# Kernel optimization log

Measured on AMD Instinct MI355X. Metric: run time of the kernel, lower is better.

## Reference

```python
import jax, jax.numpy as jnp
import numpy as np

K = 20
EPS = 1e-5
NEG_SLOPE = 0.2


def _knn_idx(x, k):
    # x: (B, N, C). Torch: pd = -||xi||^2 + 2 xi.xj - ||xj||^2, topk largest = nearest.
    inner = jnp.einsum('bnc,bmc->bnm', x, x)
    xx = jnp.sum(x * x, axis=-1)  # (B, N)
    pd = 2.0 * inner - xx[:, :, None] - xx[:, None, :]
    _, idx = jax.lax.top_k(pd, k)  # (B, N, k)
    return idx


def _bn_lrelu(h, gamma, beta, axes):
    mean = jnp.mean(h, axis=axes)
    var = jnp.var(h, axis=axes)  # biased, as in torch BN training normalization
    hn = (h - mean) * jax.lax.rsqrt(var + EPS) * gamma + beta
    return jnp.where(hn >= 0, hn, NEG_SLOPE * hn)


def _edge_conv(x, W, gamma, beta, k):
    # x: (B, N, C); W: (O, 2C). Returns (B, N, O).
    idx = _knn_idx(x, k)
    nbr = jax.vmap(lambda xb, ib: xb[ib])(x, idx)  # (B, N, k, C) gather
    center = jnp.broadcast_to(x[:, :, None, :], nbr.shape)
    edge = jnp.concatenate([nbr - center, center], axis=-1)  # (B, N, k, 2C)
    h = jnp.einsum('bnkc,oc->bnko', edge, W)
    h = _bn_lrelu(h, gamma, beta, axes=(0, 1, 2))
    return jnp.max(h, axis=2)  # max over k -> (B, N, O)


def setup_inputs() -> dict:
    key = jax.random.key(0)
    ks = jax.random.split(key, 16)
    B, N = 32, 1024
    d = {'x': jax.random.normal(ks[0], (B, N, 3), dtype=jnp.float32)}
    dims = [(64, 6), (64, 128), (128, 128), (256, 256), (1024, 512)]
    for i, (o, c) in enumerate(dims, start=1):
        d[f'W{i}'] = jax.random.normal(ks[i], (o, c), dtype=jnp.float32) * 0.05
        d[f'g{i}'] = jnp.ones((o,), dtype=jnp.float32)
        d[f'b{i}'] = jnp.zeros((o,), dtype=jnp.float32)
    return d


def reference(x, W1, g1, b1, W2, g2, b2, W3, g3, b3, W4, g4, b4, W5, g5, b5):
    B = x.shape[0]
    x1 = _edge_conv(x, W1, g1, b1, K)    # (B, N, 64)
    x2 = _edge_conv(x1, W2, g2, b2, K)   # (B, N, 64)
    x3 = _edge_conv(x2, W3, g3, b3, K)   # (B, N, 128)
    x4 = _edge_conv(x3, W4, g4, b4, K)   # (B, N, 256)
    cat = jnp.concatenate([x1, x2, x3, x4], axis=-1)  # (B, N, 512)
    h = jnp.einsum('bnc,oc->bno', cat, W5)            # (B, N, 1024)
    h = _bn_lrelu(h, g5, b5, axes=(0, 1))
    out = jnp.max(h, axis=1)  # adaptive max pool over points -> (B, 1024)
    return out.reshape(B, 1, -1)
```

## Files before the change

### kernel.cpp

```cpp
#include <hip/hip_runtime.h>
#include <math.h>

#define BB 32
#define NN 1024
#define KNNK 20
#define PTS (BB*NN)

typedef __attribute__((ext_vector_type(8)))  short short8;
typedef __attribute__((ext_vector_type(4)))  float f32x4;
typedef __attribute__((ext_vector_type(16))) float f32x16;

__device__ __forceinline__ float lrelu(float v){ return v >= 0.f ? v : 0.2f*v; }

__device__ __forceinline__ unsigned short f2b(float x){
    union { float f; unsigned u; } c; c.f = x;
    unsigned r = c.u + 0x7FFFu + ((c.u >> 16) & 1u);
    return (unsigned short)(r >> 16);
}

__global__ void sq_kernel(const float* __restrict__ x, int stride, int C, float* __restrict__ xx){
    int pn = blockIdx.x*256 + threadIdx.x;
    if (pn >= PTS) return;
    const float* r = x + (size_t)pn*stride;
    float s = 0.f;
    if ((C & 3) == 0){
        for (int c = 0; c < C; c += 4){
            float4 v = *(const float4*)&r[c];
            s = fmaf(v.x, v.x, s); s = fmaf(v.y, v.y, s);
            s = fmaf(v.z, v.z, s); s = fmaf(v.w, v.w, s);
        }
    } else {
        for (int c = 0; c < C; ++c){ float v = r[c]; s = fmaf(v, v, s); }
    }
    xx[pn] = s;
}

template<int C>
__global__ void __launch_bounds__(512, 4) knn_kernel(const float* __restrict__ x, int stride,
                                                     const float* __restrict__ xx,
                                                     int* __restrict__ idxout){
    constexpr int KC = 8;
    __shared__ __align__(16) float Bs[2][NN][4];
    __shared__ float xs[NN];
    int bid = (int)blockIdx.x;
    bid = (bid & 7)*128 + (bid >> 3);
    const int b  = bid >> 5;
    const int rb = bid & 31;
    const int r0 = rb * 32;
    const int tid = threadIdx.x;
    const int wv = tid >> 6, lane = tid & 63;
    const float* xb = x + (size_t)b*NN*stride;

    if (tid < 256) *(float4*)&xs[tid*4] = *(const float4*)&xx[b*NN + tid*4];

    float acc[4][16];
    #pragma unroll
    for (int r=0;r<4;++r)
        #pragma unroll
        for (int q=0;q<16;++q) acc[r][q] = 0.f;

    const int wrow = wv*4;

    #pragma unroll 1
    for (int kc = 0; kc < C; kc += KC){
        __syncthreads();
        #pragma unroll
        for (int ps = 0; ps < 4; ++ps){
            int i = tid + ps*512;
            int col = i >> 1, half = i & 1;
            float4 v;
            if constexpr (C == 3){
                float vv[4];
                #pragma unroll
                for (int j = 0; j < 4; ++j){
                    int k = half*4 + j;
                    vv[j] = (k < 3) ? xb[(size_t)col*3 + k] : 0.f;
                }
                v = make_float4(vv[0], vv[1], vv[2], vv[3]);
            } else {
                v = *(const float4*)&xb[(size_t)col*stride + kc + half*4];
            }
            *(float4*)&Bs[half][col][0] = v;
        }
        __syncthreads();
        #pragma unroll
        for (int s = 0; s < 2; ++s){
            float4 ar[4];
            #pragma unroll
            for (int r=0;r<4;++r)
                ar[r] = *(const float4*)&Bs[s][r0 + wrow + r][0];
            #pragma unroll
            for (int q=0;q<16;++q){
                float4 bv = *(const float4*)&Bs[s][lane + 64*q][0];
                #pragma unroll
                for (int r=0;r<4;++r){
                    acc[r][q] = fmaf(ar[r].x, bv.x, acc[r][q]);
                    acc[r][q] = fmaf(ar[r].y, bv.y, acc[r][q]);
                    acc[r][q] = fmaf(ar[r].z, bv.z, acc[r][q]);
                    acc[r][q] = fmaf(ar[r].w, bv.w, acc[r][q]);
                }
            }
        }
    }

    const unsigned long long lt = (lane == 0) ? 0ull : ((~0ull) >> (64 - lane));
    #pragma unroll
    for (int r = 0; r < 4; ++r){
        const int lrow = r0 + wrow + r;
        const float xi = xs[lrow];
        unsigned u[16];
        #pragma unroll
        for (int q = 0; q < 16; ++q){
            float d = 2.f*acc[r][q] - xi - xs[lane + 64*q];
            unsigned bits = __float_as_uint(d);
            unsigned m = (bits & 0x80000000u) ? 0xFFFFFFFFu : 0x80000000u;
            u[q] = bits ^ m;
        }
        unsigned t = 0u;
        for (int bb = 31; bb >= 0; --bb){
            unsigned cand = t | (1u << bb);
            int cnt = 0;
            #pragma unroll
            for (int q = 0; q < 16; ++q)
                cnt += (int)__popcll(__ballot(u[q] >= cand));
            if (cnt >= KNNK) t = cand;
        }
        int* orow = idxout + ((size_t)b*NN + lrow) * KNNK;
        int cbase = 0;
        #pragma unroll
        for (int q = 0; q < 16; ++q){
            bool gt2 = (u[q] > t);
            unsigned long long mask = __ballot(gt2);
            if (gt2) orow[cbase + (int)__popcll(mask & lt)] = q*64 + lane;
            cbase += (int)__popcll(mask);
        }
        #pragma unroll
        for (int q = 0; q < 16; ++q){
            bool eq = (u[q] == t);
            unsigned long long mask = __ballot(eq);
            int pos = cbase + (int)__popcll(mask & lt);
            if (eq && pos < KNNK) orow[pos] = q*64 + lane;
            cbase += (int)__popcll(mask);
        }
    }
}

template<int C, int O>
__global__ void __launch_bounds__(256) gemmG_kernel(const float* __restrict__ x, int stride,
                                                    const float* __restrict__ W,
                                                    float* __restrict__ G1, float* __restrict__ Gd){
    constexpr int KC = (C < 32 ? C : 32);
    __shared__ float Xl [KC][68];
    __shared__ float W1l[KC][68];
    __shared__ float W2l[KC][68];
    const int tid = threadIdx.x;
    const int r0 = blockIdx.x * 64;
    const int o0 = blockIdx.y * 64;
    const int rt = tid & 15, ct = tid >> 4;

    float a1[4][4] = {{0.f}}, a2[4][4] = {{0.f}};
    for (int kc = 0; kc < C; kc += KC){
        __syncthreads();
        for (int i = tid; i < KC*64; i += 256){
            int k = i % KC, rr = i / KC;
            Xl [k][rr] = x[(size_t)(r0+rr)*stride + kc + k];
            W1l[k][rr] = W[(size_t)(o0+rr)*(2*C) + kc + k];
            W2l[k][rr] = W[(size_t)(o0+rr)*(2*C) + C + kc + k];
        }
        __syncthreads();
        #pragma unroll
        for (int k = 0; k < KC; ++k){
            float4 xa = *(const float4*)&Xl [k][rt*4];
            float4 w1 = *(const float4*)&W1l[k][ct*4];
            float4 w2 = *(const float4*)&W2l[k][ct*4];
            float xv[4] = {xa.x, xa.y, xa.z, xa.w};
            #pragma unroll
            for (int i = 0; i < 4; ++i){
                a1[i][0] = fmaf(xv[i], w1.x, a1[i][0]);
                a1[i][1] = fmaf(xv[i], w1.y, a1[i][1]);
                a1[i][2] = fmaf(xv[i], w1.z, a1[i][2]);
                a1[i][3] = fmaf(xv[i], w1.w, a1[i][3]);
                a2[i][0] = fmaf(xv[i], w2.x, a2[i][0]);
                a2[i][1] = fmaf(xv[i], w2.y, a2[i][1]);
                a2[i][2] = fmaf(xv[i], w2.z, a2[i][2]);
                a2[i][3] = fmaf(xv[i], w2.w, a2[i][3]);
            }
        }
    }
    #pragma unroll
    for (int i = 0; i < 4; ++i){
        size_t row = (size_t)(r0 + rt*4 + i);
        float4 g1v = make_float4(a1[i][0], a1[i][1], a1[i][2], a1[i][3]);
        float4 gdv = make_float4(a2[i][0]-a1[i][0], a2[i][1]-a1[i][1],
                                 a2[i][2]-a1[i][2], a2[i][3]-a1[i][3]);
        *(float4*)&G1[row*O + o0 + ct*4] = g1v;
        *(float4*)&Gd[row*O + o0 + ct*4] = gdv;
    }
}

template<int O>
__global__ void __launch_bounds__(256) gather_kernel(const float* __restrict__ G1,
                                                     const float* __restrict__ Gd,
                                                     const int* __restrict__ idxg, int bgbase,
                                                     float* __restrict__ catslice,
                                                     float* __restrict__ stats){
    constexpr int OG = O/4;
    constexpr int PP = 256/OG;
    constexpr int NP = 16;
    __shared__ int nbs[NP][KNNK];
    const int nwg = (int)gridDim.x;
    int bid = (int)blockIdx.x;
    if ((nwg & 7) == 0){
        const int cpx = nwg >> 3;
        bid = (bid & 7) * cpx + (bid >> 3);
    }
    const int tid = threadIdx.x;
    const int p0 = bid * NP;
    for (int i = tid; i < NP*KNNK; i += 256){
        int pp = i / KNNK, kk = i - pp*KNNK;
        int pl = p0 + pp;
        nbs[pp][kk] = ((pl >> 10) << 10) + idxg[(size_t)(bgbase + pl)*KNNK + kk];
    }
    __syncthreads();
    const int o4 = (tid % OG)*4;
    const int pq = tid / OG;
    float S1[4] = {0.f,0.f,0.f,0.f}, S2[4] = {0.f,0.f,0.f,0.f};
    for (int pp = pq; pp < NP; pp += PP){
        int pl = p0 + pp;
        float4 dv = *(const float4*)&Gd[(size_t)pl*O + o4];
        float d[4] = {dv.x, dv.y, dv.z, dv.w};
        float mx[4] = {-INFINITY,-INFINITY,-INFINITY,-INFINITY};
        float ls[4] = {0.f,0.f,0.f,0.f}, lq[4] = {0.f,0.f,0.f,0.f};
        #pragma unroll
        for (int kk = 0; kk < KNNK; ++kk){
            float4 gv = *(const float4*)&G1[(size_t)nbs[pp][kk]*O + o4];
            float ga[4] = {gv.x, gv.y, gv.z, gv.w};
            #pragma unroll
            for (int c = 0; c < 4; ++c){
                mx[c] = fmaxf(mx[c], ga[c]);
                ls[c] += ga[c];
                lq[c] = fmaf(ga[c], ga[c], lq[c]);
            }
        }
        float4 outv;
        float* op = &outv.x;
        #pragma unroll
        for (int c = 0; c < 4; ++c){
            S1[c] += ls[c] + 20.f*d[c];
            S2[c] += lq[c] + 2.f*d[c]*ls[c] + 20.f*d[c]*d[c];
            op[c] = mx[c] + d[c];
        }
        *(float4*)&catslice[(size_t)(bgbase + pl)*512 + o4] = outv;
    }
    int rep = bid & 63;
    #pragma unroll
    for (int c = 0; c < 4; ++c){
        atomicAdd(&stats[rep*2*O + o4 + c],     S1[c]);
        atomicAdd(&stats[rep*2*O + O + o4 + c], S2[c]);
    }
}

__global__ void fin_kernel(const float* __restrict__ stats, int O, float cnt,
                           float* __restrict__ mean, float* __restrict__ invstd){
    int o = threadIdx.x;
    if (o >= O) return;
    float s1 = 0.f, s2 = 0.f;
    for (int r = 0; r < 64; ++r){
        s1 += stats[r*2*O + o];
        s2 += stats[r*2*O + O + o];
    }
    float m = s1 / cnt;
    float v = s2 / cnt - m*m;
    mean[o] = m;
    invstd[o] = rsqrtf(v + 1e-5f);
}

template<int O>
__global__ void apply_kernel(float* __restrict__ catslice,
                             const float* __restrict__ mean, const float* __restrict__ invstd,
                             const float* __restrict__ g, const float* __restrict__ bt){
    int i = blockIdx.x*256 + threadIdx.x;
    int pn = i / O, o = i - pn*O;
    float* p = &catslice[(size_t)pn*512 + o];
    float hn = (*p - mean[o]) * invstd[o] * g[o] + bt[o];
    *p = lrelu(hn);
}

__global__ void tob16_kernel(const float* __restrict__ src, unsigned short* __restrict__ dst, int n4){
    int i = blockIdx.x*256 + threadIdx.x;
    if (i >= n4) return;
    float4 v = *(const float4*)&src[(size_t)i*4];
    ushort4 o;
    o.x = f2b(v.x); o.y = f2b(v.y); o.z = f2b(v.z); o.w = f2b(v.w);
    *(ushort4*)&dst[(size_t)i*4] = o;
}

__global__ void __launch_bounds__(256) l5m_kernel(const unsigned short* __restrict__ Am,
                                                  const unsigned short* __restrict__ Bm,
                                                  float* __restrict__ pmax,
                                                  float* __restrict__ psum,
                                                  float* __restrict__ psq){
    __shared__ __align__(16) unsigned short As[128][64];
    __shared__ __align__(16) unsigned short Bs[128][64];
    const int tid = threadIdx.x;
    const int r0 = blockIdx.x * 128;
    const int o0 = blockIdx.y * 128;
    const int w = tid >> 6, lane = tid & 63;
    const int m32 = lane & 31, kh = lane >> 5;
    const int wm = (w & 1) * 64;
    const int wn = (w >> 1) * 64;

    f32x16 acc[2][2];
    #pragma unroll
    for (int i=0;i<2;++i)
        #pragma unroll
        for (int j=0;j<2;++j)
            #pragma unroll
            for (int r=0;r<16;++r) acc[i][j][r] = 0.f;

    for (int kc = 0; kc < 512; kc += 64){
        __syncthreads();
        #pragma unroll
        for (int t = 0; t < 4; ++t){
            int i = tid + t*256;
            int rr = i >> 3, ch = i & 7;
            int sl = ch ^ (rr & 7);
            *(uint4*)&As[rr][sl*8] = *(const uint4*)&Am[(size_t)(r0+rr)*512 + kc + ch*8];
            *(uint4*)&Bs[rr][sl*8] = *(const uint4*)&Bm[(size_t)(o0+rr)*512 + kc + ch*8];
        }
        __syncthreads();
        #pragma unroll
        for (int q = 0; q < 4; ++q){
            int lk = q*2 + kh;
            short8 a[2], bfr[2];
            #pragma unroll
            for (int mb = 0; mb < 2; ++mb){
                int rA = wm + mb*32 + m32;
                a[mb] = *(const short8*)&As[rA][(lk ^ (rA & 7))*8];
            }
            #pragma unroll
            for (int nb = 0; nb < 2; ++nb){
                int rB = wn + nb*32 + m32;
                bfr[nb] = *(const short8*)&Bs[rB][(lk ^ (rB & 7))*8];
            }
            #pragma unroll
            for (int mb = 0; mb < 2; ++mb)
                #pragma unroll
                for (int nb = 0; nb < 2; ++nb)
                    acc[mb][nb] = __builtin_amdgcn_mfma_f32_32x32x16_bf16(a[mb], bfr[nb], acc[mb][nb], 0, 0, 0);
        }
    }
    __syncthreads();
    float* red = (float*)&As[0][0];
    #pragma unroll
    for (int nb = 0; nb < 2; ++nb){
        float mx = -INFINITY, s1 = 0.f, s2 = 0.f;
        #pragma unroll
        for (int mb = 0; mb < 2; ++mb)
            #pragma unroll
            for (int r = 0; r < 16; ++r){
                float v = acc[mb][nb][r];
                mx = fmaxf(mx, v); s1 += v; s2 = fmaf(v, v, s2);
            }
        mx = fmaxf(mx, __shfl_xor(mx, 32));
        s1 += __shfl_xor(s1, 32);
        s2 += __shfl_xor(s2, 32);
        if (lane < 32){
            int col = wn + nb*32 + m32;
            float* p = red + ((size_t)(w & 1) * 128 + col) * 3;
            p[0] = mx; p[1] = s1; p[2] = s2;
        }
    }
    __syncthreads();
    if (tid < 128){
        const float* p0 = red + (size_t)tid*3;
        const float* p1 = red + (size_t)(128 + tid)*3;
        float mx = fmaxf(p0[0], p1[0]);
        float s1 = p0[1] + p1[1];
        float s2 = p0[2] + p1[2];
        size_t pi = (size_t)blockIdx.x*1024 + o0 + tid;
        pmax[pi] = mx; psum[pi] = s1; psq[pi] = s2;
    }
}

__global__ void fin5_kernel(const float* __restrict__ pmax, const float* __restrict__ psum,
                            const float* __restrict__ psq,
                            const float* __restrict__ g, const float* __restrict__ bt,
                            float* __restrict__ out){
    int o = blockIdx.x*256 + threadIdx.x;
    float s1 = 0.f, s2 = 0.f;
    for (int r = 0; r < 256; ++r){
        s1 += psum[(size_t)r*1024 + o];
        s2 += psq [(size_t)r*1024 + o];
    }
    float m  = s1 / 32768.f;
    float v  = s2 / 32768.f - m*m;
    float is = rsqrtf(v + 1e-5f);
    float gg = g[o], bb2 = bt[o];
    for (int b = 0; b < 32; ++b){
        float mx = -INFINITY;
        #pragma unroll
        for (int ns = 0; ns < 8; ++ns) mx = fmaxf(mx, pmax[((size_t)b*8 + ns)*1024 + o]);
        float hn = (mx - m) * is * gg + bb2;
        out[(size_t)b*1024 + o] = lrelu(hn);
    }
}

extern "C" void kernel_launch(void* const* d_in, const int* in_sizes, int n_in,
                              void* d_out, int out_size, void* d_ws, size_t ws_size,
                              hipStream_t stream) {
    (void)in_sizes; (void)n_in; (void)out_size;
    const float* x  = (const float*)d_in[0];
    const float* W1 = (const float*)d_in[1];  const float* g1 = (const float*)d_in[2];  const float* b1 = (const float*)d_in[3];
    const float* W2 = (const float*)d_in[4];  const float* g2 = (const float*)d_in[5];  const float* b2 = (const float*)d_in[6];
    const float* W3 = (const float*)d_in[7];  const float* g3 = (const float*)d_in[8];  const float* b3 = (const float*)d_in[9];
    const float* W4 = (const float*)d_in[10]; const float* g4 = (const float*)d_in[11]; const float* b4 = (const float*)d_in[12];
    const float* W5 = (const float*)d_in[13]; const float* g5 = (const float*)d_in[14]; const float* b5 = (const float*)d_in[15];
    float* out = (float*)d_out;

    const size_t fixedBytes = (size_t)PTS*512*4 + (size_t)PTS*KNNK*4 + (size_t)PTS*4
                            + (size_t)64*2*256*4 + 2048*4 + 3*(size_t)256*1024*4
                            + (size_t)1024*512*2;
    int CB;
    if      (ws_size >= fixedBytes + (size_t)32*NN*NN*4) CB = 32;
    else if (ws_size >= fixedBytes + (size_t)16*NN*NN*4) CB = 16;
    else                                                 CB = 8;
    const size_t Rbytes = (size_t)CB*NN*NN*4;

    char* wsp = (char*)d_ws;
    float* cat    = (float*)wsp; wsp += (size_t)PTS*512*4;
    char*  R      = wsp;         wsp += Rbytes;
    int*   idx    = (int*)  wsp; wsp += (size_t)PTS*KNNK*4;
    float* xx     = (float*)wsp; wsp += (size_t)PTS*4;
    float* stats  = (float*)wsp; wsp += (size_t)64*2*256*4;
    float* mean   = (float*)wsp; wsp += 1024*4;
    float* invstd = (float*)wsp; wsp += 1024*4;
    float* pmax   = (float*)wsp; wsp += (size_t)256*1024*4;
    float* psum   = (float*)wsp; wsp += (size_t)256*1024*4;
    float* psq    = (float*)wsp; wsp += (size_t)256*1024*4;
    unsigned short* W5b = (unsigned short*)wsp; wsp += (size_t)1024*512*2;

    float* G1    = (float*)R;
    float* GdS   = (float*)(R + (size_t)16*1024*1024);
    float* GdB   = (float*)(R + (size_t)32*1024*1024);
    unsigned short* catB = (unsigned short*)R;

    const float cntE = (float)(PTS*KNNK);
    const bool bigG = (Rbytes >= (size_t)64*1024*1024);

    sq_kernel<<<PTS/256, 256, 0, stream>>>(x, 3, 3, xx);
    knn_kernel<3><<<1024, 512, 0, stream>>>(x, 3, xx, idx);
    hipMemsetAsync(stats, 0, 64*2*256*4, stream);
    gemmG_kernel<3,64><<<dim3(512,1), 256, 0, stream>>>(x, 3, W1, G1, GdS);
    gather_kernel<64><<<2048, 256, 0, stream>>>(G1, GdS, idx, 0, cat + 0, stats);
    fin_kernel<<<1, 64, 0, stream>>>(stats, 64, cntE, mean, invstd);
    apply_kernel<64><<<PTS*64/256, 256, 0, stream>>>(cat + 0, mean, invstd, g1, b1);

    sq_kernel<<<PTS/256, 256, 0, stream>>>(cat + 0, 512, 64, xx);
    knn_kernel<64><<<1024, 512, 0, stream>>>(cat + 0, 512, xx, idx);
    hipMemsetAsync(stats, 0, 64*2*256*4, stream);
    gemmG_kernel<64,64><<<dim3(512,1), 256, 0, stream>>>(cat + 0, 512, W2, G1, GdS);
    gather_kernel<64><<<2048, 256, 0, stream>>>(G1, GdS, idx, 0, cat + 64, stats);
    fin_kernel<<<1, 64, 0, stream>>>(stats, 64, cntE, mean, invstd);
    apply_kernel<64><<<PTS*64/256, 256, 0, stream>>>(cat + 64, mean, invstd, g2, b2);

    sq_kernel<<<PTS/256, 256, 0, stream>>>(cat + 64, 512, 64, xx);
    knn_kernel<64><<<1024, 512, 0, stream>>>(cat + 64, 512, xx, idx);
    hipMemsetAsync(stats, 0, 64*2*256*4, stream);
    gemmG_kernel<64,128><<<dim3(512,2), 256, 0, stream>>>(cat + 64, 512, W3, G1, GdS);
    gather_kernel<128><<<2048, 256, 0, stream>>>(G1, GdS, idx, 0, cat + 128, stats);
    fin_kernel<<<1, 128, 0, stream>>>(stats, 128, cntE, mean, invstd);
    apply_kernel<128><<<PTS*128/256, 256, 0, stream>>>(cat + 128, mean, invstd, g3, b3);

    sq_kernel<<<PTS/256, 256, 0, stream>>>(cat + 128, 512, 128, xx);
    knn_kernel<128><<<1024, 512, 0, stream>>>(cat + 128, 512, xx, idx);
    hipMemsetAsync(stats, 0, 64*2*256*4, stream);
    if (bigG){
        gemmG_kernel<128,256><<<dim3(512,4), 256, 0, stream>>>(cat + 128, 512, W4, G1, GdB);
        gather_kernel<256><<<2048, 256, 0, stream>>>(G1, GdB, idx, 0, cat + 256, stats);
    } else {
        for (int bg = 0; bg < 4; ++bg){
            gemmG_kernel<128,256><<<dim3(128,4), 256, 0, stream>>>(cat + 128 + (size_t)bg*8192*512, 512, W4, G1, GdS);
            gather_kernel<256><<<512, 256, 0, stream>>>(G1, GdS, idx, bg*8192, cat + 256, stats);
        }
    }
    fin_kernel<<<1, 256, 0, stream>>>(stats, 256, cntE, mean, invstd);
    apply_kernel<256><<<PTS*256/256, 256, 0, stream>>>(cat + 256, mean, invstd, g4, b4);

    tob16_kernel<<<PTS*512/4/256, 256, 0, stream>>>(cat, catB, PTS*512/4);
    tob16_kernel<<<1024*512/4/256, 256, 0, stream>>>(W5, W5b, 1024*512/4);
    l5m_kernel<<<dim3(256, 8), 256, 0, stream>>>(catB, W5b, pmax, psum, psq);
    fin5_kernel<<<4, 256, 0, stream>>>(pmax, psum, psq, g5, b5, out);
}
```

Baseline: 1.331 ms.

## Stage per-batch G1 column slice in LDS for neighbor gather

Replaces the edge-conv gather kernel with a version that loads one batch's 1024-row by 32-column slice of G1 into shared memory (about 147 KB). Each block then serves all 1024 points of that batch over 16 passes, reading neighbor rows from LDS instead of global memory. BN statistics are first reduced within each wave with shuffles, so fewer atomics are issued. The cost is far fewer blocks (as few as 64 for the 64-channel layers) and very low occupancy because of the large LDS footprint, which can leave most CUs idle.

```diff
diff --git a/kernel.cpp b/kernel.cpp
--- a/kernel.cpp
+++ b/kernel.cpp
@@ -199,41 +199,45 @@
 }
 
 template<int O>
-__global__ void __launch_bounds__(256) gather_kernel(const float* __restrict__ G1,
-                                                     const float* __restrict__ Gd,
-                                                     const int* __restrict__ idxg, int bgbase,
-                                                     float* __restrict__ catslice,
-                                                     float* __restrict__ stats){
-    constexpr int OG = O/4;
-    constexpr int PP = 256/OG;
-    constexpr int NP = 16;
-    __shared__ int nbs[NP][KNNK];
-    const int nwg = (int)gridDim.x;
-    int bid = (int)blockIdx.x;
-    if ((nwg & 7) == 0){
-        const int cpx = nwg >> 3;
-        bid = (bid & 7) * cpx + (bid >> 3);
-    }
+__global__ void __launch_bounds__(512) gatherB_kernel(const float* __restrict__ G1,
+                                                      const float* __restrict__ Gd,
+                                                      const int* __restrict__ idxg, int bgbase,
+                                                      float* __restrict__ catslice,
+                                                      float* __restrict__ stats){
+    __shared__ __align__(16) float G1s[1024][36];
+    __shared__ int nbs[64][KNNK];
+    const int bl = blockIdx.x;
+    const int cc = blockIdx.y * 32;
     const int tid = threadIdx.x;
-    const int p0 = bid * NP;
-    for (int i = tid; i < NP*KNNK; i += 256){
-        int pp = i / KNNK, kk = i - pp*KNNK;
-        int pl = p0 + pp;
-        nbs[pp][kk] = ((pl >> 10) << 10) + idxg[(size_t)(bgbase + pl)*KNNK + kk];
-    }
-    __syncthreads();
-    const int o4 = (tid % OG)*4;
-    const int pq = tid / OG;
+    const size_t prow = (size_t)bl*1024;
+
+    for (int i = tid; i < 8192; i += 512){
+        int row = i >> 3, q8 = i & 7;
+        float4 v = *(const float4*)&G1[(prow + row)*O + cc + q8*4];
+        *(float4*)&G1s[row][q8*4] = v;
+    }
+
+    const int c4 = (tid & 7)*4;
+    const int pq = tid >> 3;
+    const int lane = tid & 63;
     float S1[4] = {0.f,0.f,0.f,0.f}, S2[4] = {0.f,0.f,0.f,0.f};
-    for (int pp = pq; pp < NP; pp += PP){
-        int pl = p0 + pp;
-        float4 dv = *(const float4*)&Gd[(size_t)pl*O + o4];
+
+    for (int ps = 0; ps < 16; ++ps){
+        __syncthreads();
+        for (int i = tid; i < 64*KNNK; i += 512){
+            int pp = i / KNNK, kk = i - (i/KNNK)*KNNK;
+            nbs[pp][kk] = idxg[((size_t)bgbase + prow + ps*64 + pp)*KNNK + kk];
+        }
+        __syncthreads();
+        const int p = ps*64 + pq;
+        float4 dv = *(const float4*)&Gd[(prow + p)*O + cc + c4];
         float d[4] = {dv.x, dv.y, dv.z, dv.w};
         float mx[4] = {-INFINITY,-INFINITY,-INFINITY,-INFINITY};
         float ls[4] = {0.f,0.f,0.f,0.f}, lq[4] = {0.f,0.f,0.f,0.f};
         #pragma unroll
         for (int kk = 0; kk < KNNK; ++kk){
-            float4 gv = *(const float4*)&G1[(size_t)nbs[pp][kk]*O + o4];
+            int row = nbs[pq][kk];
+            float4 gv = *(const float4*)&G1s[row][c4];
             float ga[4] = {gv.x, gv.y, gv.z, gv.w};
             #pragma unroll
             for (int c = 0; c < 4; ++c){
@@ -250,13 +254,24 @@
             S2[c] += lq[c] + 2.f*d[c]*ls[c] + 20.f*d[c]*d[c];
             op[c] = mx[c] + d[c];
         }
-        *(float4*)&catslice[(size_t)(bgbase + pl)*512 + o4] = outv;
-    }
-    int rep = bid & 63;
+        *(float4*)&catslice[((size_t)bgbase + prow + p)*512 + cc + c4] = outv;
+    }
+
     #pragma unroll
     for (int c = 0; c < 4; ++c){
-        atomicAdd(&stats[rep*2*O + o4 + c],     S1[c]);
-        atomicAdd(&stats[rep*2*O + O + o4 + c], S2[c]);
+        #pragma unroll
+        for (int m = 8; m < 64; m <<= 1){
+            S1[c] += __shfl_xor(S1[c], m);
+            S2[c] += __shfl_xor(S2[c], m);
+        }
+    }
+    if (lane < 8){
+        int rep = ((int)blockIdx.x*8 + (int)blockIdx.y) & 63;
+        #pragma unroll
+        for (int c = 0; c < 4; ++c){
+            atomicAdd(&stats[rep*2*O + cc + lane*4 + c],     S1[c]);
+            atomicAdd(&stats[rep*2*O + O + cc + lane*4 + c], S2[c]);
+        }
     }
 }
 
@@ -452,7 +467,7 @@
     knn_kernel<3><<<1024, 512, 0, stream>>>(x, 3, xx, idx);
     hipMemsetAsync(stats, 0, 64*2*256*4, stream);
     gemmG_kernel<3,64><<<dim3(512,1), 256, 0, stream>>>(x, 3, W1, G1, GdS);
-    gather_kernel<64><<<2048, 256, 0, stream>>>(G1, GdS, idx, 0, cat + 0, stats);
+    gatherB_kernel<64><<<dim3(32,2), 512, 0, stream>>>(G1, GdS, idx, 0, cat + 0, stats);
     fin_kernel<<<1, 64, 0, stream>>>(stats, 64, cntE, mean, invstd);
     apply_kernel<64><<<PTS*64/256, 256, 0, stream>>>(cat + 0, mean, invstd, g1, b1);
 
@@ -460,7 +475,7 @@
     knn_kernel<64><<<1024, 512, 0, stream>>>(cat + 0, 512, xx, idx);
     hipMemsetAsync(stats, 0, 64*2*256*4, stream);
     gemmG_kernel<64,64><<<dim3(512,1), 256, 0, stream>>>(cat + 0, 512, W2, G1, GdS);
-    gather_kernel<64><<<2048, 256, 0, stream>>>(G1, GdS, idx, 0, cat + 64, stats);
+    gatherB_kernel<64><<<dim3(32,2), 512, 0, stream>>>(G1, GdS, idx, 0, cat + 64, stats);
     fin_kernel<<<1, 64, 0, stream>>>(stats, 64, cntE, mean, invstd);
     apply_kernel<64><<<PTS*64/256, 256, 0, stream>>>(cat + 64, mean, invstd, g2, b2);
 
@@ -468,7 +483,7 @@
     knn_kernel<64><<<1024, 512, 0, stream>>>(cat + 64, 512, xx, idx);
     hipMemsetAsync(stats, 0, 64*2*256*4, stream);
     gemmG_kernel<64,128><<<dim3(512,2), 256, 0, stream>>>(cat + 64, 512, W3, G1, GdS);
-    gather_kernel<128><<<2048, 256, 0, stream>>>(G1, GdS, idx, 0, cat + 128, stats);
+    gatherB_kernel<128><<<dim3(32,4), 512, 0, stream>>>(G1, GdS, idx, 0, cat + 128, stats);
     fin_kernel<<<1, 128, 0, stream>>>(stats, 128, cntE, mean, invstd);
     apply_kernel<128><<<PTS*128/256, 256, 0, stream>>>(cat + 128, mean, invstd, g3, b3);
 
@@ -477,11 +492,11 @@
     hipMemsetAsync(stats, 0, 64*2*256*4, stream);
     if (bigG){
         gemmG_kernel<128,256><<<dim3(512,4), 256, 0, stream>>>(cat + 128, 512, W4, G1, GdB);
-        gather_kernel<256><<<2048, 256, 0, stream>>>(G1, GdB, idx, 0, cat + 256, stats);
+        gatherB_kernel<256><<<dim3(32,8), 512, 0, stream>>>(G1, GdB, idx, 0, cat + 256, stats);
     } else {
         for (int bg = 0; bg < 4; ++bg){
             gemmG_kernel<128,256><<<dim3(128,4), 256, 0, stream>>>(cat + 128 + (size_t)bg*8192*512, 512, W4, G1, GdS);
-            gather_kernel<256><<<512, 256, 0, stream>>>(G1, GdS, idx, bg*8192, cat + 256, stats);
+            gatherB_kernel<256><<<dim3(8,8), 512, 0, stream>>>(G1, GdS, idx, bg*8192, cat + 256, stats);
         }
     }
     fin_kernel<<<1, 256, 0, stream>>>(stats, 256, cntE, mean, invstd);
```

Result: faster. 1.229 ms (-7.6%).
